# Kernel tuning notes

Hardware: AMD Instinct MI355X
Metric: run time of the kernel (lower is better)

Reference implementation:

```python
import jax, jax.numpy as jnp
import numpy as np
from jax import lax

K = 3       # kernel_conv
STRIDE = 1
PAD = 1


def setup_inputs() -> dict:
    key = jax.random.key(0)
    ks = jax.random.split(key, 11)
    b, n, H, W = 8, 64, 128, 128
    m = 64
    kk = K * K
    return {
        "x": jax.random.normal(ks[0], (b, n, H, W), jnp.float32),
        "atw1": jax.random.uniform(ks[1], (b, kk, H, W), jnp.float32),  # sigmoid-range attention1 output
        "weight": jax.random.normal(ks[2], (m, n, K, K), jnp.float32) * 0.05,
        "a2_w1": jax.random.normal(ks[3], (kk, n), jnp.float32) * 0.1,
        "a2_b1": jax.random.normal(ks[4], (kk,), jnp.float32) * 0.1,
        "a2_w2": jax.random.normal(ks[5], (kk, kk), jnp.float32) * 0.1,
        "a2_b2": jax.random.normal(ks[6], (kk,), jnp.float32) * 0.1,
        "a3_w1": jax.random.normal(ks[7], (m, n), jnp.float32) * 0.1,
        "a3_b1": jax.random.normal(ks[8], (m,), jnp.float32) * 0.1,
        "a3_w2": jax.random.normal(ks[9], (m, m), jnp.float32) * 0.1,
        "a3_b2": jax.random.normal(ks[10], (m,), jnp.float32) * 0.1,
    }


def reference(x, atw1, weight, a2_w1, a2_b1, a2_w2, a2_b2, a3_w1, a3_b1, a3_w2, a3_b2):
    b, n, H, W = x.shape
    m = weight.shape[0]
    kk = K * K
    n_H = 1 + (H + 2 * PAD - K) // STRIDE
    n_W = 1 + (W + 2 * PAD - K) // STRIDE
    P = n_H * n_W

    # F.unfold(x, k, stride, padding): [b, n*k*k, P] with channel-major ordering (c, kh, kw)
    patches = lax.conv_general_dilated_patches(
        x, (K, K), (STRIDE, STRIDE), [(PAD, PAD), (PAD, PAD)])  # [b, n*kk, n_H, n_W]
    kx = patches.reshape(b, n, kk, P)

    # attention2: global avg pool + two 1x1 convs -> per-batch per-tap ratio [b, kk]
    g = x.mean(axis=(2, 3))                                   # [b, n]
    ratio = jax.nn.relu(g @ a2_w1.T + a2_b1) @ a2_w2.T + a2_b2  # [b, kk]

    # per-pixel per-tap weight (broadcast over input channels, as the torch repeat/view does)
    a = atw1.reshape(b, kk, P) * ratio[:, :, None]            # [b, kk, P]
    wx = kx * a[:, None, :, :]                                # [b, n, kk, P]

    # dynamic-weighted im2col matmul with static conv weight
    w = weight.reshape(m, n, kk)
    y = jnp.einsum('bctp,mct->bmp', wx, w)                    # [b, m, P]

    # attention3 bias: global avg pool + two 1x1 convs -> [b, m]
    bias = jax.nn.relu(g @ a3_w1.T + a3_b1) @ a3_w2.T + a3_b2
    y = y + bias[:, :, None]

    # F.fold with kernel 1 is a reshape back to the spatial grid
    return y.reshape(b, m, n_H, n_W)
```

## Files before the change

### kernel.cpp

```cpp
#include <hip/hip_runtime.h>

typedef __attribute__((ext_vector_type(8))) short short8;
typedef __attribute__((ext_vector_type(4))) float f32x4;

#define HH 128
#define WW 128
#define TW 16
#define TH 4
#define HALOW 18
#define HALOH 6
#define NPIX (HALOW * HALOH)
#define NA (9 * TH * TW)

typedef __attribute__((address_space(1))) const unsigned int glds_src_t;
typedef __attribute__((address_space(3))) unsigned int glds_dst_t;

__device__ inline unsigned short f2bf(float f) {
    unsigned int u = __builtin_bit_cast(unsigned int, f);
    u += 0x7fffu + ((u >> 16) & 1u);
    return (unsigned short)(u >> 16);
}

__global__ __launch_bounds__(256) void prep_kernel(
    const float* __restrict__ x, const float* __restrict__ wgt,
    unsigned short* __restrict__ xT, float* __restrict__ partials,
    unsigned short* __restrict__ W3, float* __restrict__ zpage) {
    const int id = blockIdx.x;
    const int tid = threadIdx.x;
    if (id == 0 && tid < 32) zpage[tid] = 0.f;
    {
        int i = id * 256 + tid;
        if (i < 64 * 64 * 9) {
            int j = i & 7, rest = i >> 3;
            int m = rest & 63; rest >>= 6;
            int lk = rest & 3; rest >>= 2;
            int ks = rest & 1, t = rest >> 1;
            int c = ks * 32 + lk * 8 + j;
            W3[i] = f2bf(wgt[(m * 64 + c) * 9 + t]);
        }
    }
    const int b = id & 7, pt = id >> 3;
    const int p0 = pt * 64;
    __shared__ unsigned int lt[64 * 33];
    __shared__ float red[8][32][2];

    const int px = tid & 63, cp0 = tid >> 6;
    const float* xb = x + (size_t)b * 64 * (HH * WW) + p0 + px;
    #pragma unroll
    for (int i = 0; i < 8; ++i) {
        int cp = cp0 + 4 * i;
        float v0 = xb[(size_t)(2 * cp) * (HH * WW)];
        float v1 = xb[(size_t)(2 * cp + 1) * (HH * WW)];
        lt[px * 33 + cp] = (unsigned)f2bf(v0) | ((unsigned)f2bf(v1) << 16);
    }
    __syncthreads();
    #pragma unroll
    for (int it = 0; it < 2; ++it) {
        int idx = it * 256 + tid;
        int p = idx >> 3, ch = idx & 7;
        int o = p * 33 + ch * 4;
        uint4 v = make_uint4(lt[o], lt[o + 1], lt[o + 2], lt[o + 3]);
        *(uint4*)(xT + ((size_t)(b * (HH * WW) + p0 + p) * 64 + ch * 8)) = v;
    }
    {
        int cp = tid & 31, grp = tid >> 5;
        float s0 = 0.f, s1 = 0.f;
        #pragma unroll
        for (int j2 = 0; j2 < 8; ++j2) {
            unsigned u = lt[(grp * 8 + j2) * 33 + cp];
            s0 += __builtin_bit_cast(float, u << 16);
            s1 += __builtin_bit_cast(float, u & 0xffff0000u);
        }
        red[grp][cp][0] = s0;
        red[grp][cp][1] = s1;
    }
    __syncthreads();
    if (tid < 64) {
        float s = 0.f;
        #pragma unroll
        for (int g2 = 0; g2 < 8; ++g2) s += red[g2][tid >> 1][tid & 1];
        partials[(size_t)(b * 256 + pt) * 64 + tid] = s;
    }
}

__global__ __launch_bounds__(256, 2) void main_kernel(
    const unsigned short* __restrict__ xT, const float* __restrict__ atw1,
    const unsigned short* __restrict__ W3, const float* __restrict__ partials,
    const float* __restrict__ a2w1, const float* __restrict__ a2b1,
    const float* __restrict__ a2w2, const float* __restrict__ a2b2,
    const float* __restrict__ a3w1, const float* __restrict__ a3b1,
    const float* __restrict__ a3w2, const float* __restrict__ a3b2,
    float* __restrict__ out, const float* __restrict__ zpage) {
    const int id = blockIdx.x;
    const int b = id & 7;
    const int j = id >> 3;
    const int tid = threadIdx.x;
    const int lane = tid & 63;
    const int wtile = tid >> 6;
    const int lm = lane & 15;
    const int lk = lane >> 4;

    __shared__ char xsc[2][16384];
    __shared__ float alds[2][768];
    __shared__ float rb[4][64];
    __shared__ float gs[64], h3[64], h2[12], rrs[12], bbs[64];

    const char* xbb = (const char*)(xT + (size_t)b * (HH * WW) * 64);
    const float* ab = atw1 + (size_t)b * 9 * (HH * WW);
    float* ob = out + (size_t)b * 64 * (HH * WW);
    const char* zp = (const char*)zpage;

    auto STAGE = [&](int bi, int task) {
        const int py0 = (task >> 3) * TH, px0 = (task & 7) * TW;
        #pragma unroll
        for (int i = 0; i < 4; ++i) {
            int idx = i * 256 + tid;
            int pix = idx >> 3, ch = idx & 7;
            int yy = pix / HALOW;
            int xx = pix - yy * HALOW;
            int gy = py0 + yy - 1, gx = px0 + xx - 1;
            bool ok = (pix < NPIX) && (gy >= 0) && (gy < HH) && (gx >= 0) && (gx < WW);
            const char* src = ok
                ? xbb + (((size_t)(gy * WW + gx)) << 7) + ((ch * 16) ^ ((pix & 7) << 4))
                : zp;
            char* dst = &xsc[bi][(i * 256 + wtile * 64) * 16];
            __builtin_amdgcn_global_load_lds((glds_src_t*)src, (glds_dst_t*)dst, 16, 0, 0);
        }
        #pragma unroll
        for (int i = 0; i < 3; ++i) {
            int idx = i * 256 + tid;
            int t = idx >> 6, rem = idx & 63;
            int rr = rem >> 4, cc = rem & 15;
            bool ok = idx < NA;
            const char* src = ok
                ? (const char*)(ab + (size_t)t * (HH * WW) + (py0 + rr) * WW + px0 + cc)
                : zp;
            float* dst = &alds[bi][i * 256 + wtile * 64];
            __builtin_amdgcn_global_load_lds((glds_src_t*)src, (glds_dst_t*)dst, 4, 0, 0);
        }
    };

    STAGE(0, j * 4);

    short8 wfrag[9][2];
    {
        const short8* W3v = (const short8*)W3;
        #pragma unroll
        for (int t = 0; t < 9; ++t)
            #pragma unroll
            for (int ks = 0; ks < 2; ++ks)
                wfrag[t][ks] = W3v[(((t * 2 + ks) * 4 + lk) * 64) + wtile * 16 + lm];
    }

    {
        const int t = tid & 63, is = tid >> 6;
        float s = 0.f;
        #pragma unroll 8
        for (int k = 0; k < 64; ++k)
            s += partials[(size_t)(b * 256 + is + 4 * k) * 64 + t];
        rb[is][t] = s;
        __syncthreads();
        if (tid < 64)
            gs[t] = (rb[0][t] + rb[1][t] + rb[2][t] + rb[3][t]) * (1.f / (HH * WW));
        __syncthreads();
        if (tid < 64) {
            float s3 = 0.f;
            #pragma unroll 8
            for (int i = 0; i < 64; ++i) s3 += gs[i] * a3w1[t * 64 + i];
            h3[t] = fmaxf(s3 + a3b1[t], 0.f);
            if (t < 9) {
                float s2 = 0.f;
                #pragma unroll 8
                for (int i = 0; i < 64; ++i) s2 += gs[i] * a2w1[t * 64 + i];
                h2[t] = fmaxf(s2 + a2b1[t], 0.f);
            }
        }
        __syncthreads();
        if (tid < 64) {
            float o = 0.f;
            #pragma unroll 8
            for (int i = 0; i < 64; ++i) o += h3[i] * a3w2[t * 64 + i];
            bbs[t] = o + a3b2[t];
            if (t < 9) {
                float r = 0.f;
                #pragma unroll
                for (int i = 0; i < 9; ++i) r += h2[i] * a2w2[t * 9 + i];
                rrs[t] = r + a2b2[t];
            }
        }
        __syncthreads();
    }

    float rat[9];
    #pragma unroll
    for (int t = 0; t < 9; ++t) rat[t] = rrs[t];
    float biasr[4];
    #pragma unroll
    for (int q = 0; q < 4; ++q) biasr[q] = bbs[wtile * 16 + lk * 4 + q];

    #pragma unroll 1
    for (int it = 0; it < 4; ++it) {
        if (it < 3) {
            STAGE((it + 1) & 1, j * 4 + it + 1);
            __builtin_amdgcn_sched_barrier(0);
        }

        const int task = j * 4 + it;
        const int py0 = (task >> 3) * TH, px0 = (task & 7) * TW;
        const char* xs = xsc[it & 1];
        const float* al = alds[it & 1];

        float av[4][9];
        #pragma unroll
        for (int r = 0; r < 4; ++r)
            #pragma unroll
            for (int t = 0; t < 9; ++t)
                av[r][t] = al[t * 64 + r * 16 + lm] * rat[t];

        f32x4 yac[4];
        #pragma unroll
        for (int r = 0; r < 4; ++r) yac[r] = (f32x4){0.f, 0.f, 0.f, 0.f};

        #pragma unroll
        for (int hl = 0; hl < 6; ++hl) {
            const int pixr = hl * HALOW + lm;
            short8 bf[3][2];
            #pragma unroll
            for (int dx = 0; dx < 3; ++dx) {
                const int pix = pixr + dx;
                const int sw = (pix & 7) << 4;
                const char* bp2 = xs + pix * 128;
                #pragma unroll
                for (int ks = 0; ks < 2; ++ks)
                    bf[dx][ks] = __builtin_bit_cast(short8,
                        *(const uint4*)(bp2 + ((ks * 64 + lk * 16) ^ sw)));
            }
            #pragma unroll
            for (int dy = 0; dy < 3; ++dy) {
                const int r = hl - dy;
                if (r < 0 || r > 3) continue;
                #pragma unroll
                for (int dx = 0; dx < 3; ++dx) {
                    const int t = dy * 3 + dx;
                    f32x4 z = {0.f, 0.f, 0.f, 0.f};
                    z = __builtin_amdgcn_mfma_f32_16x16x32_bf16(wfrag[t][0], bf[dx][0], z, 0, 0, 0);
                    z = __builtin_amdgcn_mfma_f32_16x16x32_bf16(wfrag[t][1], bf[dx][1], z, 0, 0, 0);
                    #pragma unroll
                    for (int q = 0; q < 4; ++q) yac[r][q] = fmaf(av[r][t], z[q], yac[r][q]);
                }
            }
        }
        #pragma unroll
        for (int r = 0; r < 4; ++r) {
            const int pyg = py0 + r;
            #pragma unroll
            for (int q = 0; q < 4; ++q) {
                int m = wtile * 16 + lk * 4 + q;
                ob[((size_t)m * HH + pyg) * WW + px0 + lm] = yac[r][q] + biasr[q];
            }
        }

        if (it < 3) {
            asm volatile("s_waitcnt vmcnt(16)" ::: "memory");
            __builtin_amdgcn_s_barrier();
            __builtin_amdgcn_sched_barrier(0);
        }
    }
}

extern "C" void kernel_launch(void* const* d_in, const int* in_sizes, int n_in,
                              void* d_out, int out_size, void* d_ws, size_t ws_size,
                              hipStream_t stream) {
    const float* x    = (const float*)d_in[0];
    const float* atw1 = (const float*)d_in[1];
    const float* wgt  = (const float*)d_in[2];
    const float* a2w1 = (const float*)d_in[3];
    const float* a2b1 = (const float*)d_in[4];
    const float* a2w2 = (const float*)d_in[5];
    const float* a2b2 = (const float*)d_in[6];
    const float* a3w1 = (const float*)d_in[7];
    const float* a3b1 = (const float*)d_in[8];
    const float* a3w2 = (const float*)d_in[9];
    const float* a3b2 = (const float*)d_in[10];
    float* out = (float*)d_out;

    float* ws = (float*)d_ws;
    float* zpage = ws + 640;
    unsigned short* W3 = (unsigned short*)(ws + 1024);
    float* partials = ws + 19456;
    unsigned short* xT = (unsigned short*)(ws + 150528);

    prep_kernel<<<dim3(2048), dim3(256), 0, stream>>>(x, wgt, xT, partials, W3, zpage);
    main_kernel<<<dim3(512), dim3(256), 0, stream>>>(
        xT, atw1, W3, partials, a2w1, a2b1, a2w2, a2b2,
        a3w1, a3b1, a3w2, a3b2, out, zpage);
}
```

Before: 37.50 us.

## Give each wave a private LDS tile buffer and split work across twice the blocks

After: 55.90 us. +49.1%, slower.

```diff
diff --git a/kernel.cpp b/kernel.cpp
--- a/kernel.cpp
+++ b/kernel.cpp
@@ -10,6 +10,7 @@
 #define HALOW 18
 #define HALOH 6
 #define NPIX (HALOW * HALOH)
+#define XSLOTS 896
 #define NA (9 * TH * TW)
 
 typedef __attribute__((address_space(1))) const unsigned int glds_src_t;
@@ -96,12 +97,12 @@
     const int j = id >> 3;
     const int tid = threadIdx.x;
     const int lane = tid & 63;
-    const int wtile = tid >> 6;
+    const int w = tid >> 6;
     const int lm = lane & 15;
     const int lk = lane >> 4;
 
-    __shared__ char xsc[2][16384];
-    __shared__ float alds[2][768];
+    __shared__ char xsc[4][XSLOTS * 16];
+    __shared__ float alds[4][NA];
     __shared__ float rb[4][64];
     __shared__ float gs[64], h3[64], h2[12], rrs[12], bbs[64];
 
@@ -110,11 +111,14 @@
     float* ob = out + (size_t)b * 64 * (HH * WW);
     const char* zp = (const char*)zpage;
 
-    auto STAGE = [&](int bi, int task) {
-        const int py0 = (task >> 3) * TH, px0 = (task & 7) * TW;
-        #pragma unroll
-        for (int i = 0; i < 4; ++i) {
-            int idx = i * 256 + tid;
+    char* xw = xsc[w];
+    float* aw = alds[w];
+
+    auto STAGE = [&](int tile) {
+        const int py0 = (tile >> 3) * TH, px0 = (tile & 7) * TW;
+        #pragma unroll
+        for (int i = 0; i < 14; ++i) {
+            int idx = i * 64 + lane;
             int pix = idx >> 3, ch = idx & 7;
             int yy = pix / HALOW;
             int xx = pix - yy * HALOW;
@@ -123,24 +127,22 @@
             const char* src = ok
                 ? xbb + (((size_t)(gy * WW + gx)) << 7) + ((ch * 16) ^ ((pix & 7) << 4))
                 : zp;
-            char* dst = &xsc[bi][(i * 256 + wtile * 64) * 16];
+            char* dst = xw + i * 64 * 16;
             __builtin_amdgcn_global_load_lds((glds_src_t*)src, (glds_dst_t*)dst, 16, 0, 0);
         }
         #pragma unroll
-        for (int i = 0; i < 3; ++i) {
-            int idx = i * 256 + tid;
+        for (int i = 0; i < 9; ++i) {
+            int idx = i * 64 + lane;
             int t = idx >> 6, rem = idx & 63;
             int rr = rem >> 4, cc = rem & 15;
-            bool ok = idx < NA;
-            const char* src = ok
-                ? (const char*)(ab + (size_t)t * (HH * WW) + (py0 + rr) * WW + px0 + cc)
-                : zp;
-            float* dst = &alds[bi][i * 256 + wtile * 64];
+            const char* src =
+                (const char*)(ab + (size_t)t * (HH * WW) + (py0 + rr) * WW + px0 + cc);
+            float* dst = aw + i * 64;
             __builtin_amdgcn_global_load_lds((glds_src_t*)src, (glds_dst_t*)dst, 4, 0, 0);
         }
     };
 
-    STAGE(0, j * 4);
+    STAGE(2 * j);
 
     short8 wfrag[9][2];
     {
@@ -149,7 +151,7 @@
         for (int t = 0; t < 9; ++t)
             #pragma unroll
             for (int ks = 0; ks < 2; ++ks)
-                wfrag[t][ks] = W3v[(((t * 2 + ks) * 4 + lk) * 64) + wtile * 16 + lm];
+                wfrag[t][ks] = W3v[(((t * 2 + ks) * 4 + lk) * 64) + w * 16 + lm];
     }
 
     {
@@ -196,26 +198,19 @@
     for (int t = 0; t < 9; ++t) rat[t] = rrs[t];
     float biasr[4];
     #pragma unroll
-    for (int q = 0; q < 4; ++q) biasr[q] = bbs[wtile * 16 + lk * 4 + q];
+    for (int q = 0; q < 4; ++q) biasr[q] = bbs[w * 16 + lk * 4 + q];
 
     #pragma unroll 1
-    for (int it = 0; it < 4; ++it) {
-        if (it < 3) {
-            STAGE((it + 1) & 1, j * 4 + it + 1);
-            __builtin_amdgcn_sched_barrier(0);
-        }
-
-        const int task = j * 4 + it;
-        const int py0 = (task >> 3) * TH, px0 = (task & 7) * TW;
-        const char* xs = xsc[it & 1];
-        const float* al = alds[it & 1];
+    for (int s = 0; s < 2; ++s) {
+        const int tile = 2 * j + s;
+        const int py0 = (tile >> 3) * TH, px0 = (tile & 7) * TW;
 
         float av[4][9];
         #pragma unroll
         for (int r = 0; r < 4; ++r)
             #pragma unroll
             for (int t = 0; t < 9; ++t)
-                av[r][t] = al[t * 64 + r * 16 + lm] * rat[t];
+                av[r][t] = aw[t * 64 + r * 16 + lm] * rat[t];
 
         f32x4 yac[4];
         #pragma unroll
@@ -229,7 +224,7 @@
             for (int dx = 0; dx < 3; ++dx) {
                 const int pix = pixr + dx;
                 const int sw = (pix & 7) << 4;
-                const char* bp2 = xs + pix * 128;
+                const char* bp2 = xw + pix * 128;
                 #pragma unroll
                 for (int ks = 0; ks < 2; ++ks)
                     bf[dx][ks] = __builtin_bit_cast(short8,
@@ -255,14 +250,16 @@
             const int pyg = py0 + r;
             #pragma unroll
             for (int q = 0; q < 4; ++q) {
-                int m = wtile * 16 + lk * 4 + q;
+                int m = w * 16 + lk * 4 + q;
                 ob[((size_t)m * HH + pyg) * WW + px0 + lm] = yac[r][q] + biasr[q];
             }
         }
 
-        if (it < 3) {
-            asm volatile("s_waitcnt vmcnt(16)" ::: "memory");
-            __builtin_amdgcn_s_barrier();
+        if (s == 0) {
+            asm volatile("s_waitcnt lgkmcnt(0)" ::: "memory");
+            __builtin_amdgcn_sched_barrier(0);
+            STAGE(2 * j + 1);
+            asm volatile("s_waitcnt vmcnt(0)" ::: "memory");
             __builtin_amdgcn_sched_barrier(0);
         }
     }
@@ -291,7 +288,7 @@
     unsigned short* xT = (unsigned short*)(ws + 150528);
 
     prep_kernel<<<dim3(2048), dim3(256), 0, stream>>>(x, wgt, xT, partials, W3, zpage);
-    main_kernel<<<dim3(512), dim3(256), 0, stream>>>(
+    main_kernel<<<dim3(1024), dim3(256), 0, stream>>>(
         xT, atw1, W3, partials, a2w1, a2b1, a2w2, a2b2,
         a3w1, a3b1, a3w2, a3b2, out, zpage);
 }
```
